# Kernel optimization log

Measured on AMD Instinct MI355X. Metric: run time of the kernel, lower is better.

## Reference

```python
import jax, jax.numpy as jnp
import numpy as np

HEADS = 8
WH, WW = 8, 8
DIM = 256
B = 4096
N = WH * WW  # 64


def _rel_index():
    ch, cw = np.meshgrid(np.arange(WH), np.arange(WW), indexing='ij')
    coords = np.stack([ch.ravel(), cw.ravel()])  # (2, N)
    rel = coords[:, :, None] - coords[:, None, :]  # (2, N, N)
    rel = rel.transpose(1, 2, 0)
    rel[:, :, 0] += WH - 1
    rel[:, :, 1] += WW - 1
    rel[:, :, 0] *= 2 * WW - 1
    return jnp.asarray(rel.sum(-1), dtype=jnp.int32)  # (N, N)


def setup_inputs() -> dict:
    key = jax.random.key(0)
    ks = jax.random.split(key, 6)
    x = jax.random.normal(ks[0], (B, N, DIM), dtype=jnp.float32)
    attn_mask = jnp.zeros((1, HEADS, N, N), dtype=jnp.float32)
    w_qkv = jax.random.normal(ks[1], (3 * DIM, DIM), dtype=jnp.float32) * 0.02
    w_proj = jax.random.normal(ks[2], (DIM, DIM), dtype=jnp.float32) * 0.02
    b_proj = jax.random.normal(ks[3], (DIM,), dtype=jnp.float32) * 0.02
    table = jax.random.normal(ks[4], (225, HEADS), dtype=jnp.float32) * 0.02
    return {"x": x, "attn_mask": attn_mask, "w_qkv": w_qkv, "w_proj": w_proj,
            "b_proj": b_proj, "table": table, "rel_index": _rel_index()}


def reference(x, attn_mask, w_qkv, w_proj, b_proj, table, rel_index):
    Bn, Nn, C = x.shape
    hd = C // HEADS
    qkv = (x @ w_qkv.T).reshape(Bn, Nn, 3, HEADS, hd)
    q = qkv[:, :, 0].transpose(0, 2, 1, 3)  # (B,h,N,d)
    k = qkv[:, :, 1].transpose(0, 2, 1, 3)
    v = qkv[:, :, 2].transpose(0, 2, 1, 3)
    scale = 1.0 / jnp.sqrt(jnp.asarray(hd, dtype=x.dtype))
    attn = jnp.einsum('bhnd,bhmd->bhnm', q, k) * scale
    bias = table[rel_index]  # (N,N,h)
    attn = attn + bias.transpose(2, 0, 1)[None] + attn_mask
    attn = jax.nn.softmax(attn, axis=-1)
    out = jnp.einsum('bhnm,bhmd->bhnd', attn, v)
    out = out.transpose(0, 2, 1, 3).reshape(Bn, Nn, C)
    return out @ w_proj.T + b_proj
```

## Files before the change

### kernel.cpp

```cpp
#include <hip/hip_runtime.h>
#include <hip/hip_bf16.h>

#define HEADS 8
#define NTOK 64
#define DIM 256

typedef __attribute__((ext_vector_type(8))) short bf16x8;
typedef __attribute__((ext_vector_type(4))) float f32x4;
typedef unsigned short u16;

__device__ __forceinline__ u16 f2bf(float f) {
    union { float f; unsigned u; } c; c.f = f;
    unsigned u = c.u;
    unsigned rounded = u + 0x7FFF + ((u >> 16) & 1);
    return (u16)(rounded >> 16);
}

__device__ __forceinline__ float dpp_xor1(float x) {
    return __int_as_float(__builtin_amdgcn_mov_dpp(__float_as_int(x), 0xB1, 0xF, 0xF, true));
}
__device__ __forceinline__ float dpp_xor2(float x) {
    return __int_as_float(__builtin_amdgcn_mov_dpp(__float_as_int(x), 0x4E, 0xF, 0xF, true));
}

__global__ void prep_kernel(const float* __restrict__ wqkv,
                            const float* __restrict__ wproj,
                            const float* __restrict__ table,
                            const int* __restrict__ rel_index,
                            const float* __restrict__ mask,
                            u16* __restrict__ wq_bf,
                            u16* __restrict__ wp_bf,
                            float* __restrict__ bias) {
    const int NQ = 768 * 256;
    const int NP = 256 * 256;
    const int NB = HEADS * NTOK * NTOK;
    int total = NQ + NP + NB;
    for (int i = blockIdx.x * blockDim.x + threadIdx.x; i < total;
         i += gridDim.x * blockDim.x) {
        if (i < NQ) {
            wq_bf[i] = f2bf(wqkv[i]);
        } else if (i < NQ + NP) {
            wp_bf[i - NQ] = f2bf(wproj[i - NQ]);
        } else {
            int j = i - (NQ + NP);
            int h = j >> 12;
            int nm = j & 4095;
            bias[j] = table[rel_index[nm] * HEADS + h] + mask[j];
        }
    }
}

__launch_bounds__(1024, 4)
__global__ void win_attn_kernel(const float* __restrict__ x,
                                const u16* __restrict__ wq_bf,
                                const u16* __restrict__ wp_bf,
                                const float* __restrict__ bias,
                                const float* __restrict__ b_proj,
                                float* __restrict__ out) {
    __shared__ u16 smem[69120];
    u16* s_x  = smem;
    u16* s_q  = smem + 16896;
    u16* s_k  = smem + 33792;
    u16* s_vt = smem + 50688;

    const int b = blockIdx.x;
    const int tid = threadIdx.x;
    const int w = tid >> 6;
    const int l = tid & 63;
    const int l16 = l & 15;
    const int lhi = l >> 4;

    const float* xw = x + (size_t)b * (NTOK * DIM);
#pragma unroll
    for (int it = 0; it < 4; ++it) {
        int idx4 = tid + it * 1024;
        float4 v = reinterpret_cast<const float4*>(xw)[idx4];
        int row = idx4 >> 6;
        int col = (idx4 & 63) * 4;
        ushort4 o;
        o.x = f2bf(v.x); o.y = f2bf(v.y); o.z = f2bf(v.z); o.w = f2bf(v.w);
        *reinterpret_cast<ushort4*>(&s_x[row * 264 + col]) = o;
    }
    __syncthreads();

    f32x4 acc2[2][4];
    f32x4 acc1[4];
    const f32x4 zero = {0.f, 0.f, 0.f, 0.f};
#pragma unroll
    for (int j = 0; j < 2; ++j)
#pragma unroll
        for (int ct = 0; ct < 4; ++ct) acc2[j][ct] = zero;
#pragma unroll
    for (int rt = 0; rt < 4; ++rt) acc1[rt] = zero;

    const u16* wrow0 = wq_bf + ((2 * w) * 16 + l16) * 256;
    const u16* wrow1 = wrow0 + 16 * 256;
    const u16* vrow  = wq_bf + (512 + w * 16 + l16) * 256;

    bf16x8 wa0 = *reinterpret_cast<const bf16x8*>(wrow0 + lhi * 8);
    bf16x8 wa1 = *reinterpret_cast<const bf16x8*>(wrow1 + lhi * 8);
    bf16x8 wv  = *reinterpret_cast<const bf16x8*>(vrow  + lhi * 8);

    for (int ks = 0; ks < 8; ++ks) {
        const int k0 = ks * 32 + lhi * 8;
        bf16x8 xf[4];
#pragma unroll
        for (int t = 0; t < 4; ++t)
            xf[t] = *reinterpret_cast<const bf16x8*>(&s_x[(t * 16 + l16) * 264 + k0]);
        bf16x8 na0, na1, nv;
        if (ks < 7) {
            na0 = *reinterpret_cast<const bf16x8*>(wrow0 + k0 + 32);
            na1 = *reinterpret_cast<const bf16x8*>(wrow1 + k0 + 32);
            nv  = *reinterpret_cast<const bf16x8*>(vrow  + k0 + 32);
        }
#pragma unroll
        for (int ct = 0; ct < 4; ++ct)
            acc2[0][ct] = __builtin_amdgcn_mfma_f32_16x16x32_bf16(wa0, xf[ct], acc2[0][ct], 0, 0, 0);
#pragma unroll
        for (int ct = 0; ct < 4; ++ct)
            acc2[1][ct] = __builtin_amdgcn_mfma_f32_16x16x32_bf16(wa1, xf[ct], acc2[1][ct], 0, 0, 0);
#pragma unroll
        for (int rt = 0; rt < 4; ++rt)
            acc1[rt] = __builtin_amdgcn_mfma_f32_16x16x32_bf16(xf[rt], wv, acc1[rt], 0, 0, 0);
        wa0 = na0; wa1 = na1; wv = nv;
    }
    {
        u16* dst = (w < 8) ? s_q : s_k;
        const int cb0 = (2 * w) * 16 - ((w < 8) ? 0 : 256);
#pragma unroll
        for (int j = 0; j < 2; ++j) {
            int cb = cb0 + j * 16;
#pragma unroll
            for (int ct = 0; ct < 4; ++ct) {
                ushort4 o;
                o.x = f2bf(acc2[j][ct][0]); o.y = f2bf(acc2[j][ct][1]);
                o.z = f2bf(acc2[j][ct][2]); o.w = f2bf(acc2[j][ct][3]);
                *reinterpret_cast<ushort4*>(&dst[(ct * 16 + l16) * 264 + cb + lhi * 4]) = o;
            }
        }
#pragma unroll
        for (int rt = 0; rt < 4; ++rt) {
            ushort4 o;
            o.x = f2bf(acc1[rt][0]); o.y = f2bf(acc1[rt][1]);
            o.z = f2bf(acc1[rt][2]); o.w = f2bf(acc1[rt][3]);
            *reinterpret_cast<ushort4*>(&s_vt[(w * 16 + l16) * 72 + rt * 16 + lhi * 4]) = o;
        }
    }
    __syncthreads();

    {
        const int h = w >> 1;
        const int half = w & 1;
        bf16x8 vfrag[2][2], qf[2], kf[4];
#pragma unroll
        for (int dt = 0; dt < 2; ++dt)
#pragma unroll
            for (int kv = 0; kv < 2; ++kv)
                vfrag[dt][kv] = *reinterpret_cast<const bf16x8*>(
                    &s_vt[(h * 32 + dt * 16 + l16) * 72 + kv * 32 + lhi * 8]);
#pragma unroll
        for (int i = 0; i < 2; ++i) {
            int rt = half * 2 + i;
            qf[i] = *reinterpret_cast<const bf16x8*>(&s_q[(rt * 16 + l16) * 264 + h * 32 + lhi * 8]);
        }
#pragma unroll
        for (int ct = 0; ct < 4; ++ct)
            kf[ct] = *reinterpret_cast<const bf16x8*>(&s_k[(ct * 16 + l16) * 264 + h * 32 + lhi * 8]);
        __syncthreads();

        u16* Pw = smem + w * 1088;
        const float scale = 0.17677669529663687f;
        const float* biash = bias + h * 4096;

#pragma unroll
        for (int i = 0; i < 2; ++i) {
            const int rt = half * 2 + i;
            f32x4 sacc[4];
#pragma unroll
            for (int ct = 0; ct < 4; ++ct)
                sacc[ct] = __builtin_amdgcn_mfma_f32_16x16x32_bf16(qf[i], kf[ct], zero, 0, 0, 0);

            float inv_[4];
#pragma unroll
            for (int r = 0; r < 4; ++r) {
                int row = rt * 16 + lhi * 4 + r;
                float p[4];
                float sum = 0.f;
#pragma unroll
                for (int ct = 0; ct < 4; ++ct) {
                    p[ct] = __expf(sacc[ct][r] * scale + biash[row * 64 + ct * 16 + l16]);
                    sum += p[ct];
                }
                sum += dpp_xor1(sum);
                sum += dpp_xor2(sum);
                sum += __shfl_xor(sum, 4, 64);
                sum += __shfl_xor(sum, 8, 64);
                inv_[r] = 1.0f / sum;
#pragma unroll
                for (int ct = 0; ct < 4; ++ct)
                    Pw[(lhi * 4 + r) * 68 + ct * 16 + l16] = f2bf(p[ct]);
            }
            bf16x8 pa0 = *reinterpret_cast<const bf16x8*>(&Pw[l16 * 68 + lhi * 8]);
            bf16x8 pa1 = *reinterpret_cast<const bf16x8*>(&Pw[l16 * 68 + 32 + lhi * 8]);
            f32x4 oacc[2];
#pragma unroll
            for (int dt = 0; dt < 2; ++dt) {
                oacc[dt] = __builtin_amdgcn_mfma_f32_16x16x32_bf16(pa0, vfrag[dt][0], zero, 0, 0, 0);
                oacc[dt] = __builtin_amdgcn_mfma_f32_16x16x32_bf16(pa1, vfrag[dt][1], oacc[dt], 0, 0, 0);
            }
#pragma unroll
            for (int dt = 0; dt < 2; ++dt)
#pragma unroll
                for (int r = 0; r < 4; ++r) {
                    int row = rt * 16 + lhi * 4 + r;
                    s_k[row * 264 + h * 32 + dt * 16 + l16] = f2bf(oacc[dt][r] * inv_[r]);
                }
        }
    }
    __syncthreads();

    f32x4 acc3[4];
#pragma unroll
    for (int ct = 0; ct < 4; ++ct) acc3[ct] = zero;

    const u16* prow = wp_bf + (w * 16 + l16) * 256;
    bf16x8 wpf = *reinterpret_cast<const bf16x8*>(prow + lhi * 8);
    for (int ks = 0; ks < 8; ++ks) {
        const int k0 = ks * 32 + lhi * 8;
        bf16x8 nf;
        if (ks < 7) nf = *reinterpret_cast<const bf16x8*>(prow + k0 + 32);
#pragma unroll
        for (int ct = 0; ct < 4; ++ct) {
            bf16x8 of = *reinterpret_cast<const bf16x8*>(&s_k[(ct * 16 + l16) * 264 + k0]);
            acc3[ct] = __builtin_amdgcn_mfma_f32_16x16x32_bf16(wpf, of, acc3[ct], 0, 0, 0);
        }
        wpf = nf;
    }
    float* outw = out + (size_t)b * (NTOK * DIM);
    {
        float4 bp = *reinterpret_cast<const float4*>(&b_proj[w * 16 + lhi * 4]);
#pragma unroll
        for (int ct = 0; ct < 4; ++ct) {
            float4 o;
            o.x = acc3[ct][0] + bp.x;
            o.y = acc3[ct][1] + bp.y;
            o.z = acc3[ct][2] + bp.z;
            o.w = acc3[ct][3] + bp.w;
            *reinterpret_cast<float4*>(&outw[(ct * 16 + l16) * 256 + w * 16 + lhi * 4]) = o;
        }
    }
}

extern "C" void kernel_launch(void* const* d_in, const int* in_sizes, int n_in,
                              void* d_out, int out_size, void* d_ws, size_t ws_size,
                              hipStream_t stream) {
    const float* x     = (const float*)d_in[0];
    const float* mask  = (const float*)d_in[1];
    const float* wqkv  = (const float*)d_in[2];
    const float* wproj = (const float*)d_in[3];
    const float* bproj = (const float*)d_in[4];
    const float* table = (const float*)d_in[5];
    const int*   relix = (const int*)d_in[6];

    u16*   wq_bf = (u16*)d_ws;
    u16*   wp_bf = wq_bf + 768 * 256;
    float* bias  = (float*)(wp_bf + 256 * 256);

    prep_kernel<<<64, 512, 0, stream>>>(wqkv, wproj, table, relix, mask,
                                        wq_bf, wp_bf, bias);
    win_attn_kernel<<<4096, 1024, 0, stream>>>(x, wq_bf, wp_bf, bias, bproj,
                                               (float*)d_out);
}
```

Measured before the change: 412.2 us.

## Assign one head per wave and keep Q/K in registers across attention

The block shrinks from 16 to 8 waves, and each wave owns one head. That wave computes its own Q, K and V columns, so Q and K never leave registers. The MFMA output layout of the QKV GEMM is fed straight into 16x16x16 MFMAs for QK^T, which removes the Q/K shared-memory round trip and one block barrier. The trade-offs are more accumulator registers per wave (launch bounds 512,2), twice the per-wave work in the projection and attention, and fewer waves per block to hide latency.

New measurement: 532.7 us. 29.2% more time.

```diff
diff --git a/kernel.cpp b/kernel.cpp
--- a/kernel.cpp
+++ b/kernel.cpp
@@ -6,6 +6,7 @@
 #define DIM 256
 
 typedef __attribute__((ext_vector_type(8))) short bf16x8;
+typedef __attribute__((ext_vector_type(4))) short bf16x4;
 typedef __attribute__((ext_vector_type(4))) float f32x4;
 typedef unsigned short u16;
 
@@ -50,18 +51,18 @@
     }
 }
 
-__launch_bounds__(1024, 4)
+__launch_bounds__(512, 2)
 __global__ void win_attn_kernel(const float* __restrict__ x,
                                 const u16* __restrict__ wq_bf,
                                 const u16* __restrict__ wp_bf,
                                 const float* __restrict__ bias,
                                 const float* __restrict__ b_proj,
                                 float* __restrict__ out) {
-    __shared__ u16 smem[69120];
+    __shared__ u16 smem[60928];
     u16* s_x  = smem;
-    u16* s_q  = smem + 16896;
-    u16* s_k  = smem + 33792;
-    u16* s_vt = smem + 50688;
+    u16* s_vt = smem + 16896;
+    u16* s_o  = smem + 35328;
+    u16* s_p  = smem + 52224;
 
     const int b = blockIdx.x;
     const int tid = threadIdx.x;
@@ -72,8 +73,8 @@
 
     const float* xw = x + (size_t)b * (NTOK * DIM);
 #pragma unroll
-    for (int it = 0; it < 4; ++it) {
-        int idx4 = tid + it * 1024;
+    for (int it = 0; it < 8; ++it) {
+        int idx4 = tid + it * 512;
         float4 v = reinterpret_cast<const float4*>(xw)[idx4];
         int row = idx4 >> 6;
         int col = (idx4 & 63) * 4;
@@ -83,113 +84,112 @@
     }
     __syncthreads();
 
-    f32x4 acc2[2][4];
-    f32x4 acc1[4];
+    const int h = w;
+    f32x4 qacc[2][4], kacc[2][4], vacc[4][2];
     const f32x4 zero = {0.f, 0.f, 0.f, 0.f};
 #pragma unroll
-    for (int j = 0; j < 2; ++j)
-#pragma unroll
-        for (int ct = 0; ct < 4; ++ct) acc2[j][ct] = zero;
-#pragma unroll
-    for (int rt = 0; rt < 4; ++rt) acc1[rt] = zero;
-
-    const u16* wrow0 = wq_bf + ((2 * w) * 16 + l16) * 256;
-    const u16* wrow1 = wrow0 + 16 * 256;
-    const u16* vrow  = wq_bf + (512 + w * 16 + l16) * 256;
-
-    bf16x8 wa0 = *reinterpret_cast<const bf16x8*>(wrow0 + lhi * 8);
-    bf16x8 wa1 = *reinterpret_cast<const bf16x8*>(wrow1 + lhi * 8);
-    bf16x8 wv  = *reinterpret_cast<const bf16x8*>(vrow  + lhi * 8);
+    for (int ct = 0; ct < 2; ++ct)
+#pragma unroll
+        for (int tt = 0; tt < 4; ++tt) {
+            qacc[ct][tt] = zero; kacc[ct][tt] = zero; vacc[tt][ct] = zero;
+        }
+
+    const u16* rq0 = wq_bf + (h * 32 + l16) * 256;
+    const u16* rq1 = rq0 + 16 * 256;
+    const u16* rk0 = wq_bf + (256 + h * 32 + l16) * 256;
+    const u16* rk1 = rk0 + 16 * 256;
+    const u16* rv0 = wq_bf + (512 + h * 32 + l16) * 256;
+    const u16* rv1 = rv0 + 16 * 256;
+
+    bf16x8 wq0 = *reinterpret_cast<const bf16x8*>(rq0 + lhi * 8);
+    bf16x8 wq1 = *reinterpret_cast<const bf16x8*>(rq1 + lhi * 8);
+    bf16x8 wk0 = *reinterpret_cast<const bf16x8*>(rk0 + lhi * 8);
+    bf16x8 wk1 = *reinterpret_cast<const bf16x8*>(rk1 + lhi * 8);
+    bf16x8 wv0 = *reinterpret_cast<const bf16x8*>(rv0 + lhi * 8);
+    bf16x8 wv1 = *reinterpret_cast<const bf16x8*>(rv1 + lhi * 8);
 
     for (int ks = 0; ks < 8; ++ks) {
         const int k0 = ks * 32 + lhi * 8;
         bf16x8 xf[4];
 #pragma unroll
-        for (int t = 0; t < 4; ++t)
-            xf[t] = *reinterpret_cast<const bf16x8*>(&s_x[(t * 16 + l16) * 264 + k0]);
-        bf16x8 na0, na1, nv;
+        for (int tt = 0; tt < 4; ++tt)
+            xf[tt] = *reinterpret_cast<const bf16x8*>(&s_x[(tt * 16 + l16) * 264 + k0]);
+        bf16x8 nq0, nq1, nk0, nk1, nv0, nv1;
         if (ks < 7) {
-            na0 = *reinterpret_cast<const bf16x8*>(wrow0 + k0 + 32);
-            na1 = *reinterpret_cast<const bf16x8*>(wrow1 + k0 + 32);
-            nv  = *reinterpret_cast<const bf16x8*>(vrow  + k0 + 32);
-        }
-#pragma unroll
-        for (int ct = 0; ct < 4; ++ct)
-            acc2[0][ct] = __builtin_amdgcn_mfma_f32_16x16x32_bf16(wa0, xf[ct], acc2[0][ct], 0, 0, 0);
-#pragma unroll
-        for (int ct = 0; ct < 4; ++ct)
-            acc2[1][ct] = __builtin_amdgcn_mfma_f32_16x16x32_bf16(wa1, xf[ct], acc2[1][ct], 0, 0, 0);
-#pragma unroll
-        for (int rt = 0; rt < 4; ++rt)
-            acc1[rt] = __builtin_amdgcn_mfma_f32_16x16x32_bf16(xf[rt], wv, acc1[rt], 0, 0, 0);
-        wa0 = na0; wa1 = na1; wv = nv;
-    }
+            nq0 = *reinterpret_cast<const bf16x8*>(rq0 + k0 + 32);
+            nq1 = *reinterpret_cast<const bf16x8*>(rq1 + k0 + 32);
+            nk0 = *reinterpret_cast<const bf16x8*>(rk0 + k0 + 32);
+            nk1 = *reinterpret_cast<const bf16x8*>(rk1 + k0 + 32);
+            nv0 = *reinterpret_cast<const bf16x8*>(rv0 + k0 + 32);
+            nv1 = *reinterpret_cast<const bf16x8*>(rv1 + k0 + 32);
+        }
+#pragma unroll
+        for (int tt = 0; tt < 4; ++tt) {
+            qacc[0][tt] = __builtin_amdgcn_mfma_f32_16x16x32_bf16(wq0, xf[tt], qacc[0][tt], 0, 0, 0);
+            qacc[1][tt] = __builtin_amdgcn_mfma_f32_16x16x32_bf16(wq1, xf[tt], qacc[1][tt], 0, 0, 0);
+            kacc[0][tt] = __builtin_amdgcn_mfma_f32_16x16x32_bf16(wk0, xf[tt], kacc[0][tt], 0, 0, 0);
+            kacc[1][tt] = __builtin_amdgcn_mfma_f32_16x16x32_bf16(wk1, xf[tt], kacc[1][tt], 0, 0, 0);
+            vacc[tt][0] = __builtin_amdgcn_mfma_f32_16x16x32_bf16(xf[tt], wv0, vacc[tt][0], 0, 0, 0);
+            vacc[tt][1] = __builtin_amdgcn_mfma_f32_16x16x32_bf16(xf[tt], wv1, vacc[tt][1], 0, 0, 0);
+        }
+        wq0 = nq0; wq1 = nq1; wk0 = nk0; wk1 = nk1; wv0 = nv0; wv1 = nv1;
+    }
+
+    bf16x4 qf[4][2], kf[4][2];
+#pragma unroll
+    for (int tt = 0; tt < 4; ++tt)
+#pragma unroll
+        for (int ct = 0; ct < 2; ++ct) {
+            bf16x4 q, k;
+#pragma unroll
+            for (int r = 0; r < 4; ++r) {
+                q[r] = (short)f2bf(qacc[ct][tt][r]);
+                k[r] = (short)f2bf(kacc[ct][tt][r]);
+            }
+            qf[tt][ct] = q; kf[tt][ct] = k;
+        }
+#pragma unroll
+    for (int tt = 0; tt < 4; ++tt)
+#pragma unroll
+        for (int ct = 0; ct < 2; ++ct) {
+            ushort4 o;
+            o.x = f2bf(vacc[tt][ct][0]); o.y = f2bf(vacc[tt][ct][1]);
+            o.z = f2bf(vacc[tt][ct][2]); o.w = f2bf(vacc[tt][ct][3]);
+            *reinterpret_cast<ushort4*>(
+                &s_vt[(h * 32 + ct * 16 + l16) * 72 + tt * 16 + lhi * 4]) = o;
+        }
+
     {
-        u16* dst = (w < 8) ? s_q : s_k;
-        const int cb0 = (2 * w) * 16 - ((w < 8) ? 0 : 256);
-#pragma unroll
-        for (int j = 0; j < 2; ++j) {
-            int cb = cb0 + j * 16;
-#pragma unroll
-            for (int ct = 0; ct < 4; ++ct) {
-                ushort4 o;
-                o.x = f2bf(acc2[j][ct][0]); o.y = f2bf(acc2[j][ct][1]);
-                o.z = f2bf(acc2[j][ct][2]); o.w = f2bf(acc2[j][ct][3]);
-                *reinterpret_cast<ushort4*>(&dst[(ct * 16 + l16) * 264 + cb + lhi * 4]) = o;
-            }
-        }
-#pragma unroll
-        for (int rt = 0; rt < 4; ++rt) {
-            ushort4 o;
-            o.x = f2bf(acc1[rt][0]); o.y = f2bf(acc1[rt][1]);
-            o.z = f2bf(acc1[rt][2]); o.w = f2bf(acc1[rt][3]);
-            *reinterpret_cast<ushort4*>(&s_vt[(w * 16 + l16) * 72 + rt * 16 + lhi * 4]) = o;
-        }
-    }
-    __syncthreads();
-
-    {
-        const int h = w >> 1;
-        const int half = w & 1;
-        bf16x8 vfrag[2][2], qf[2], kf[4];
+        bf16x8 vfrag[2][2];
 #pragma unroll
         for (int dt = 0; dt < 2; ++dt)
 #pragma unroll
             for (int kv = 0; kv < 2; ++kv)
                 vfrag[dt][kv] = *reinterpret_cast<const bf16x8*>(
                     &s_vt[(h * 32 + dt * 16 + l16) * 72 + kv * 32 + lhi * 8]);
-#pragma unroll
-        for (int i = 0; i < 2; ++i) {
-            int rt = half * 2 + i;
-            qf[i] = *reinterpret_cast<const bf16x8*>(&s_q[(rt * 16 + l16) * 264 + h * 32 + lhi * 8]);
-        }
-#pragma unroll
-        for (int ct = 0; ct < 4; ++ct)
-            kf[ct] = *reinterpret_cast<const bf16x8*>(&s_k[(ct * 16 + l16) * 264 + h * 32 + lhi * 8]);
-        __syncthreads();
-
-        u16* Pw = smem + w * 1088;
+
+        u16* Pw = s_p + w * 1088;
         const float scale = 0.17677669529663687f;
         const float* biash = bias + h * 4096;
 
 #pragma unroll
-        for (int i = 0; i < 2; ++i) {
-            const int rt = half * 2 + i;
+        for (int nt = 0; nt < 4; ++nt) {
             f32x4 sacc[4];
 #pragma unroll
-            for (int ct = 0; ct < 4; ++ct)
-                sacc[ct] = __builtin_amdgcn_mfma_f32_16x16x32_bf16(qf[i], kf[ct], zero, 0, 0, 0);
-
+            for (int mt = 0; mt < 4; ++mt) {
+                sacc[mt] = __builtin_amdgcn_mfma_f32_16x16x16bf16_1k(qf[nt][0], kf[mt][0], zero, 0, 0, 0);
+                sacc[mt] = __builtin_amdgcn_mfma_f32_16x16x16bf16_1k(qf[nt][1], kf[mt][1], sacc[mt], 0, 0, 0);
+            }
             float inv_[4];
 #pragma unroll
             for (int r = 0; r < 4; ++r) {
-                int row = rt * 16 + lhi * 4 + r;
+                int row = nt * 16 + lhi * 4 + r;
                 float p[4];
                 float sum = 0.f;
 #pragma unroll
-                for (int ct = 0; ct < 4; ++ct) {
-                    p[ct] = __expf(sacc[ct][r] * scale + biash[row * 64 + ct * 16 + l16]);
-                    sum += p[ct];
+                for (int mt = 0; mt < 4; ++mt) {
+                    p[mt] = __expf(sacc[mt][r] * scale + biash[row * 64 + mt * 16 + l16]);
+                    sum += p[mt];
                 }
                 sum += dpp_xor1(sum);
                 sum += dpp_xor2(sum);
@@ -197,8 +197,8 @@
                 sum += __shfl_xor(sum, 8, 64);
                 inv_[r] = 1.0f / sum;
 #pragma unroll
-                for (int ct = 0; ct < 4; ++ct)
-                    Pw[(lhi * 4 + r) * 68 + ct * 16 + l16] = f2bf(p[ct]);
+                for (int mt = 0; mt < 4; ++mt)
+                    Pw[(lhi * 4 + r) * 68 + mt * 16 + l16] = f2bf(p[mt]);
             }
             bf16x8 pa0 = *reinterpret_cast<const bf16x8*>(&Pw[l16 * 68 + lhi * 8]);
             bf16x8 pa1 = *reinterpret_cast<const bf16x8*>(&Pw[l16 * 68 + 32 + lhi * 8]);
@@ -212,41 +212,51 @@
             for (int dt = 0; dt < 2; ++dt)
 #pragma unroll
                 for (int r = 0; r < 4; ++r) {
-                    int row = rt * 16 + lhi * 4 + r;
-                    s_k[row * 264 + h * 32 + dt * 16 + l16] = f2bf(oacc[dt][r] * inv_[r]);
+                    int row = nt * 16 + lhi * 4 + r;
+                    s_o[row * 264 + h * 32 + dt * 16 + l16] = f2bf(oacc[dt][r] * inv_[r]);
                 }
         }
     }
     __syncthreads();
 
-    f32x4 acc3[4];
-#pragma unroll
-    for (int ct = 0; ct < 4; ++ct) acc3[ct] = zero;
-
-    const u16* prow = wp_bf + (w * 16 + l16) * 256;
-    bf16x8 wpf = *reinterpret_cast<const bf16x8*>(prow + lhi * 8);
+    f32x4 acc3[2][4];
+#pragma unroll
+    for (int t = 0; t < 2; ++t)
+#pragma unroll
+        for (int tt = 0; tt < 4; ++tt) acc3[t][tt] = zero;
+
+    const u16* prow0 = wp_bf + (w * 16 + l16) * 256;
+    const u16* prow1 = wp_bf + ((w + 8) * 16 + l16) * 256;
+    bf16x8 wp0 = *reinterpret_cast<const bf16x8*>(prow0 + lhi * 8);
+    bf16x8 wp1 = *reinterpret_cast<const bf16x8*>(prow1 + lhi * 8);
     for (int ks = 0; ks < 8; ++ks) {
         const int k0 = ks * 32 + lhi * 8;
-        bf16x8 nf;
-        if (ks < 7) nf = *reinterpret_cast<const bf16x8*>(prow + k0 + 32);
-#pragma unroll
-        for (int ct = 0; ct < 4; ++ct) {
-            bf16x8 of = *reinterpret_cast<const bf16x8*>(&s_k[(ct * 16 + l16) * 264 + k0]);
-            acc3[ct] = __builtin_amdgcn_mfma_f32_16x16x32_bf16(wpf, of, acc3[ct], 0, 0, 0);
-        }
-        wpf = nf;
+        bf16x8 np0, np1;
+        if (ks < 7) {
+            np0 = *reinterpret_cast<const bf16x8*>(prow0 + k0 + 32);
+            np1 = *reinterpret_cast<const bf16x8*>(prow1 + k0 + 32);
+        }
+#pragma unroll
+        for (int tt = 0; tt < 4; ++tt) {
+            bf16x8 of = *reinterpret_cast<const bf16x8*>(&s_o[(tt * 16 + l16) * 264 + k0]);
+            acc3[0][tt] = __builtin_amdgcn_mfma_f32_16x16x32_bf16(wp0, of, acc3[0][tt], 0, 0, 0);
+            acc3[1][tt] = __builtin_amdgcn_mfma_f32_16x16x32_bf16(wp1, of, acc3[1][tt], 0, 0, 0);
+        }
+        wp0 = np0; wp1 = np1;
     }
     float* outw = out + (size_t)b * (NTOK * DIM);
-    {
-        float4 bp = *reinterpret_cast<const float4*>(&b_proj[w * 16 + lhi * 4]);
-#pragma unroll
-        for (int ct = 0; ct < 4; ++ct) {
+#pragma unroll
+    for (int t = 0; t < 2; ++t) {
+        int colb = (w + t * 8) * 16 + lhi * 4;
+        float4 bp = *reinterpret_cast<const float4*>(&b_proj[colb]);
+#pragma unroll
+        for (int tt = 0; tt < 4; ++tt) {
             float4 o;
-            o.x = acc3[ct][0] + bp.x;
-            o.y = acc3[ct][1] + bp.y;
-            o.z = acc3[ct][2] + bp.z;
-            o.w = acc3[ct][3] + bp.w;
-            *reinterpret_cast<float4*>(&outw[(ct * 16 + l16) * 256 + w * 16 + lhi * 4]) = o;
+            o.x = acc3[t][tt][0] + bp.x;
+            o.y = acc3[t][tt][1] + bp.y;
+            o.z = acc3[t][tt][2] + bp.z;
+            o.w = acc3[t][tt][3] + bp.w;
+            *reinterpret_cast<float4*>(&outw[(tt * 16 + l16) * 256 + colb]) = o;
         }
     }
 }
@@ -268,6 +278,6 @@
 
     prep_kernel<<<64, 512, 0, stream>>>(wqkv, wproj, table, relix, mask,
                                         wq_bf, wp_bf, bias);
-    win_attn_kernel<<<4096, 1024, 0, stream>>>(x, wq_bf, wp_bf, bias, bproj,
-                                               (float*)d_out);
-}
+    win_attn_kernel<<<4096, 512, 0, stream>>>(x, wq_bf, wp_bf, bias, bproj,
+                                              (float*)d_out);
+}
```
